# Kernel optimization log

Hardware: AMD Instinct MI355X
Metric: run time of the kernel (lower is better)

The kernel has to match this reference:

```python
import jax, jax.numpy as jnp
import numpy as np

B, S, D = 2, 2048, 1024
H, DK = 16, 64            # n_heads, d_k = d_model // n_heads
EXP = 4                   # pattern-separation expand_factor
ED = DK * EXP             # expanded_dim = 256
TOPK = 32                 # top-k kept after ReLU expansion
ALPHA = 0.05
TNT = 1.0                 # trace_norm_target


def setup_inputs() -> dict:
    key = jax.random.key(0)
    ks = jax.random.split(key, 8)
    sc = 1.0 / np.sqrt(D)
    x = jax.random.normal(ks[0], (B, S, D), jnp.float32)
    W_q = jax.random.normal(ks[1], (D, D), jnp.float32) * sc
    W_k = jax.random.normal(ks[2], (D, D), jnp.float32) * sc
    W_v = jax.random.normal(ks[3], (D, D), jnp.float32) * sc
    W_o = jax.random.normal(ks[4], (D, D), jnp.float32) * sc
    # trace buffers (non-zero so the trace read path actually matters)
    traces = jax.random.normal(ks[5], (H, DK, DK), jnp.float32) * 0.02
    value_traces = jax.random.normal(ks[6], (H, ED, DK), jnp.float32) * 0.02
    # frozen random expansion projection (dentate gyrus), W / sqrt(d_k)
    W_expand = jax.random.normal(ks[7], (DK, ED), jnp.float32) / np.sqrt(DK)
    return dict(x=x, W_q=W_q, W_k=W_k, W_v=W_v, W_o=W_o,
                traces=traces, value_traces=value_traces, W_expand=W_expand)


def _eff_alpha(T):
    # alpha / (1 + ||T_h||_F / trace_norm_target), shape (1, H, 1, 1)
    norms = jnp.sqrt(jnp.sum(T * T, axis=(1, 2)))
    return (ALPHA / (1.0 + norms / TNT)).reshape(1, -1, 1, 1)


def _forward(x, W_q, W_k, W_v, W_o, traces, value_traces, W_expand):
    b, s, d = x.shape
    def proj(W):
        return jnp.einsum('bsd,de->bse', x, W).reshape(b, s, H, DK).transpose(0, 2, 1, 3)
    Q, K, V = proj(W_q), proj(W_k), proj(W_v)  # (B, H, S, DK)

    scores = jnp.einsum('bhqd,bhkd->bhqk', Q, K)
    # score trace bias: alpha_eff * (Q @ T @ K^T)
    QT = jnp.einsum('bhqd,hde->bhqe', Q, traces)
    trace_scores = jnp.einsum('bhqe,bhke->bhqk', QT, K)
    scores = (scores + _eff_alpha(traces) * trace_scores) / np.sqrt(DK)
    A = jax.nn.softmax(scores, axis=-1)
    out = jnp.einsum('bhqk,bhkd->bhqd', A, V)

    # value trace read with use_key_q shift: address with previous token's Q
    Q_addr = jnp.concatenate([jnp.zeros_like(Q[:, :, :1, :]), Q[:, :, :-1, :]], axis=2)
    # pattern separation: frozen random expansion + ReLU + top-k sparsify
    Q_exp = jax.nn.relu(jnp.einsum('bhsd,de->bhse', Q_addr, W_expand))  # (B,H,S,ED)
    kth = jax.lax.top_k(Q_exp, TOPK)[0][..., -1:]
    Q_sparse = jnp.where(Q_exp >= kth, Q_exp, 0.0)  # == scatter of top-k vals (ties at 0 contribute 0)
    stored = jnp.einsum('bhse,hed->bhsd', Q_sparse, value_traces)
    out = out + _eff_alpha(value_traces) * stored

    out = out.transpose(0, 2, 1, 3).reshape(b, s, d)
    return jnp.einsum('bsd,de->bse', out, W_o)


def reference(x, W_q, W_k, W_v, W_o, traces, value_traces, W_expand):
    return _forward(x, W_q, W_k, W_v, W_o, traces, value_traces, W_expand)
```

## Files before the change

kernel.cpp:

```cpp
#include <hip/hip_runtime.h>
#include <stdint.h>

#define Bn 2
#define Sn 2048
#define Dn 1024
#define Hn 16
#define DKn 64
#define EDn 256

typedef __attribute__((ext_vector_type(8))) short bvec8;
typedef __attribute__((ext_vector_type(4))) float fvec4;

#define MFMA(a, b, c) __builtin_amdgcn_mfma_f32_16x16x32_bf16(a, b, c, 0, 0, 0)

__device__ __forceinline__ float b2f(unsigned short u) {
  return __uint_as_float(((unsigned)u) << 16);
}
__device__ __forceinline__ unsigned short f2b(float x) {
  unsigned u = __float_as_uint(x);
  u += 0x7fffu + ((u >> 16) & 1u);
  return (unsigned short)(u >> 16);
}
__device__ __forceinline__ void g2l(const unsigned short* g, unsigned short* l) {
  __builtin_amdgcn_global_load_lds(
      (const __attribute__((address_space(1))) void*)g,
      (__attribute__((address_space(3))) void*)l, 16, 0, 0);
}
__device__ __forceinline__ int dpp_sum16(int x) {
  x += __builtin_amdgcn_update_dpp(0, x, 0x140, 0xf, 0xf, true);
  x += __builtin_amdgcn_update_dpp(0, x, 0x141, 0xf, 0xf, true);
  x += __builtin_amdgcn_update_dpp(0, x, 0x1B, 0xf, 0xf, true);
  x += __builtin_amdgcn_update_dpp(0, x, 0xB1, 0xf, 0xf, true);
  return x;
}
__device__ __forceinline__ unsigned dpp_umax16(unsigned x) {
  unsigned t;
  t = (unsigned)__builtin_amdgcn_update_dpp(0, (int)x, 0x140, 0xf, 0xf, true);
  x = x > t ? x : t;
  t = (unsigned)__builtin_amdgcn_update_dpp(0, (int)x, 0x141, 0xf, 0xf, true);
  x = x > t ? x : t;
  t = (unsigned)__builtin_amdgcn_update_dpp(0, (int)x, 0x1B, 0xf, 0xf, true);
  x = x > t ? x : t;
  t = (unsigned)__builtin_amdgcn_update_dpp(0, (int)x, 0xB1, 0xf, 0xf, true);
  x = x > t ? x : t;
  return x;
}

__global__ __launch_bounds__(256) void k_alphas(
    const float* __restrict__ traces, const float* __restrict__ vtr,
    float* __restrict__ alphas) {
  int blk = blockIdx.x;
  const float* base;
  int n;
  if (blk < 16) { base = traces + blk * DKn * DKn; n = DKn * DKn; }
  else          { base = vtr + (blk - 16) * EDn * DKn; n = EDn * DKn; }
  float s = 0.f;
  for (int i = threadIdx.x; i < n; i += 256) { float v = base[i]; s += v * v; }
  __shared__ float red[256];
  red[threadIdx.x] = s;
  __syncthreads();
  for (int off = 128; off > 0; off >>= 1) {
    if (threadIdx.x < off) red[threadIdx.x] += red[threadIdx.x + off];
    __syncthreads();
  }
  if (threadIdx.x == 0) alphas[blk] = 0.05f / (1.f + sqrtf(red[0]));
}

__global__ __launch_bounds__(256) void k_trW(
    const float* __restrict__ w0, const float* __restrict__ w1,
    const float* __restrict__ w2, const float* __restrict__ w3,
    unsigned short* __restrict__ dst) {
  int z = blockIdx.z;
  const float* src = (z == 0) ? w0 : ((z == 1) ? w1 : ((z == 2) ? w2 : w3));
  unsigned short* d = dst + (size_t)z * Dn * Dn;
  __shared__ unsigned short Tl[64][72];
  int tid = threadIdx.x;
  int k0 = blockIdx.y * 64, n0 = blockIdx.x * 64;
#pragma unroll
  for (int i = 0; i < 4; ++i) {
    int q = tid + 256 * i;
    int kr = q >> 4, c4 = q & 15;
    float4 v = *(const float4*)&src[(size_t)(k0 + kr) * Dn + n0 + 4 * c4];
    ushort4 u;
    u.x = f2b(v.x); u.y = f2b(v.y); u.z = f2b(v.z); u.w = f2b(v.w);
    *(ushort4*)&Tl[kr][4 * c4] = u;
  }
  __syncthreads();
#pragma unroll
  for (int i = 0; i < 4; ++i) {
    int q = tid + 256 * i;
    int nr = q >> 4, c4 = q & 15;
    ushort4 u;
    u.x = Tl[4 * c4 + 0][nr]; u.y = Tl[4 * c4 + 1][nr];
    u.z = Tl[4 * c4 + 2][nr]; u.w = Tl[4 * c4 + 3][nr];
    *(ushort4*)&d[(size_t)(n0 + nr) * Dn + k0 + 4 * c4] = u;
  }
}

__global__ __launch_bounds__(256) void k_mkM(const float* __restrict__ tr,
                                             const float* __restrict__ alph,
                                             unsigned short* __restrict__ Mt) {
  int h = blockIdx.x;
  float a = alph[h] * 0.125f;
  const float* th = tr + (size_t)h * DKn * DKn;
  unsigned short* mh = Mt + (size_t)h * DKn * DKn;
  for (int i = threadIdx.x; i < DKn * DKn; i += 256) {
    int e = i >> 6, k = i & 63;
    float v = a * th[(size_t)k * DKn + e] + ((e == k) ? 0.125f : 0.f);
    mh[i] = f2b(v);
  }
}

__global__ __launch_bounds__(256) void k_trE(const float* __restrict__ Wexp,
                                             unsigned short* __restrict__ WexpT) {
  int e0 = blockIdx.x * 64;
  __shared__ unsigned short Tl[64][72];
  int tid = threadIdx.x;
#pragma unroll
  for (int i = 0; i < 4; ++i) {
    int q = tid + 256 * i;
    int dr = q >> 4, c4 = q & 15;
    float4 v = *(const float4*)&Wexp[(size_t)dr * EDn + e0 + 4 * c4];
    ushort4 u;
    u.x = f2b(v.x); u.y = f2b(v.y); u.z = f2b(v.z); u.w = f2b(v.w);
    *(ushort4*)&Tl[dr][4 * c4] = u;
  }
  __syncthreads();
#pragma unroll
  for (int i = 0; i < 4; ++i) {
    int q = tid + 256 * i;
    int er = q >> 4, c4 = q & 15;
    ushort4 u;
    u.x = Tl[4 * c4 + 0][er]; u.y = Tl[4 * c4 + 1][er];
    u.z = Tl[4 * c4 + 2][er]; u.w = Tl[4 * c4 + 3][er];
    *(ushort4*)&WexpT[(size_t)(e0 + er) * DKn + 4 * c4] = u;
  }
}

__global__ __launch_bounds__(256) void k_trVT(const float* __restrict__ vtr,
                                              unsigned short* __restrict__ VTt) {
  int e0 = blockIdx.x * 64;
  int h = blockIdx.y;
  const float* src = vtr + (size_t)h * EDn * DKn;
  unsigned short* dst = VTt + (size_t)h * DKn * EDn;
  __shared__ unsigned short Tl[64][72];
  int tid = threadIdx.x;
#pragma unroll
  for (int i = 0; i < 4; ++i) {
    int q = tid + 256 * i;
    int er = q >> 4, c4 = q & 15;
    float4 v = *(const float4*)&src[(size_t)(e0 + er) * DKn + 4 * c4];
    ushort4 u;
    u.x = f2b(v.x); u.y = f2b(v.y); u.z = f2b(v.z); u.w = f2b(v.w);
    *(ushort4*)&Tl[er][4 * c4] = u;
  }
  __syncthreads();
#pragma unroll
  for (int i = 0; i < 4; ++i) {
    int q = tid + 256 * i;
    int dr = q >> 4, c4 = q & 15;
    ushort4 u;
    u.x = Tl[4 * c4 + 0][dr]; u.y = Tl[4 * c4 + 1][dr];
    u.z = Tl[4 * c4 + 2][dr]; u.w = Tl[4 * c4 + 3][dr];
    *(ushort4*)&dst[(size_t)dr * EDn + e0 + 4 * c4] = u;
  }
}

__global__ __launch_bounds__(256) void k_xb(const float* __restrict__ x,
                                            unsigned short* __restrict__ xb) {
  size_t i = ((size_t)blockIdx.x * 256 + threadIdx.x) * 4;
  float4 v = *(const float4*)&x[i];
  ushort4 u;
  u.x = f2b(v.x); u.y = f2b(v.y); u.z = f2b(v.z); u.w = f2b(v.w);
  *(ushort4*)&xb[i] = u;
}

template <int MODE>
__global__ __launch_bounds__(256) void k_gemm(
    const unsigned short* __restrict__ Ab, const float* __restrict__ Af,
    const unsigned short* __restrict__ BtBase, unsigned short* __restrict__ Qb,
    unsigned short* __restrict__ Kb, unsigned short* __restrict__ VtOut,
    float* __restrict__ Cout) {
  const int z = (MODE == 0) ? blockIdx.z : 0;
  const unsigned short* Bt = BtBase + (size_t)z * Dn * Dn;
  __shared__ unsigned short As[128 * 32];
  __shared__ unsigned short Bs[128 * 32];
  const int tid = threadIdx.x;
  const int w = tid >> 6, lane = tid & 63, qd = lane >> 4, cc = lane & 15;
  const int m0 = blockIdx.y * 128, n0 = blockIdx.x * 128;
  const int mW = 64 * (w >> 1), nW = 64 * (w & 1);
  const int srow = lane >> 2;
  const int schk = 8 * ((lane & 3) ^ (srow & 3));
  const int r0 = 32 * w + srow, r1 = r0 + 16;
  fvec4 acc[4][4];
#pragma unroll
  for (int i = 0; i < 4; ++i)
#pragma unroll
    for (int j = 0; j < 4; ++j) acc[i][j] = (fvec4){0.f, 0.f, 0.f, 0.f};

  for (int k0 = 0; k0 < Dn; k0 += 32) {
    if (MODE == 0) {
      g2l(&Ab[(size_t)(m0 + r0) * Dn + k0 + schk], &As[1024 * w]);
      g2l(&Ab[(size_t)(m0 + r1) * Dn + k0 + schk], &As[1024 * w + 512]);
    } else {
#pragma unroll
      for (int i = 0; i < 4; ++i) {
        int q = tid + 256 * i;
        int row = q >> 3, c4 = q & 7;
        float4 v = *(const float4*)&Af[(size_t)(m0 + row) * Dn + k0 + 4 * c4];
        ushort4 u;
        u.x = f2b(v.x); u.y = f2b(v.y); u.z = f2b(v.z); u.w = f2b(v.w);
        *(ushort4*)&As[row * 32 + 8 * ((c4 >> 1) ^ (row & 3)) + 4 * (c4 & 1)] =
            u;
      }
    }
    g2l(&Bt[(size_t)(n0 + r0) * Dn + k0 + schk], &Bs[1024 * w]);
    g2l(&Bt[(size_t)(n0 + r1) * Dn + k0 + schk], &Bs[1024 * w + 512]);
    __syncthreads();
    bvec8 af[4], bf[4];
#pragma unroll
    for (int i = 0; i < 4; ++i) {
      int ra = mW + 16 * i + cc;
      af[i] = *(const bvec8*)&As[ra * 32 + 8 * (qd ^ (ra & 3))];
      int rb = nW + 16 * i + cc;
      bf[i] = *(const bvec8*)&Bs[rb * 32 + 8 * (qd ^ (rb & 3))];
    }
#pragma unroll
    for (int i = 0; i < 4; ++i)
#pragma unroll
      for (int j = 0; j < 4; ++j) acc[i][j] = MFMA(af[i], bf[j], acc[i][j]);
    __syncthreads();
  }
#pragma unroll
  for (int i = 0; i < 4; ++i)
#pragma unroll
    for (int j = 0; j < 4; ++j) {
      int rowb = m0 + mW + 16 * i + 4 * qd;
      int col = n0 + nW + 16 * j + cc;
      if (MODE == 0) {
        int b = rowb >> 11, s = rowb & 2047;
        int h = col >> 6, dk = col & 63;
        if (z == 2) {
          ushort4 u;
          u.x = f2b(acc[i][j][0]); u.y = f2b(acc[i][j][1]);
          u.z = f2b(acc[i][j][2]); u.w = f2b(acc[i][j][3]);
          *(ushort4*)&VtOut[(((size_t)(b * Hn + h)) * DKn + dk) * Sn + s] = u;
        } else {
          unsigned short* Cb = (z == 0) ? Qb : Kb;
#pragma unroll
          for (int r = 0; r < 4; ++r)
            Cb[(((size_t)(b * Hn + h)) * Sn + s + r) * DKn + dk] =
                f2b(acc[i][j][r]);
        }
      } else {
#pragma unroll
        for (int r = 0; r < 4; ++r)
          Cout[(size_t)(rowb + r) * Dn + col] = acc[i][j][r];
      }
    }
}

__global__ __launch_bounds__(256, 4) void k_pattsep(
    const unsigned short* __restrict__ Qb,
    const unsigned short* __restrict__ WexpT,
    const unsigned short* __restrict__ VTt,
    const float* __restrict__ alphas, float* __restrict__ AT) {
  __shared__ uint4 Ps4[4][256];
  const int tile = blockIdx.x, bh = blockIdx.y;
  const int b = bh >> 4, h = bh & 15;
  const int tid = threadIdx.x;
  const int w = tid >> 6, lane = tid & 63, qd = lane >> 4, cc = lane & 15;
  const float avt = alphas[16 + h];

  const unsigned short* vtab = VTt + (size_t)h * DKn * EDn;
  unsigned short* Pw = (unsigned short*)Ps4[w];

  const int s0 = tile * 64 + w * 16;
  bvec8 aq0 = {}, aq1 = {};
  const int srow = s0 + cc;
  if (srow > 0) {
    const unsigned short* qp = Qb + ((size_t)bh * Sn + srow - 1) * DKn;
    aq0 = *(const bvec8*)&qp[8 * qd];
    aq1 = *(const bvec8*)&qp[32 + 8 * qd];
  }
  fvec4 E[16];
#pragma unroll
  for (int j = 0; j < 16; ++j) {
    const int e = 16 * j + cc;
    const unsigned short* wr = WexpT + (size_t)e * 64;
    bvec8 b0 = *(const bvec8*)&wr[8 * qd];
    bvec8 b1 = *(const bvec8*)&wr[32 + 8 * qd];
    fvec4 zv = {0.f, 0.f, 0.f, 0.f};
    zv = MFMA(aq0, b0, zv);
    E[j] = MFMA(aq1, b1, zv);
  }
#pragma unroll
  for (int j = 0; j < 16; ++j)
#pragma unroll
    for (int r = 0; r < 4; ++r) E[j][r] = fmaxf(E[j][r], 0.f);

  float thr[4];
#pragma unroll
  for (int r = 0; r < 4; ++r) {
    unsigned mx = 0u;
#pragma unroll
    for (int j = 0; j < 16; ++j) {
      unsigned e = __float_as_uint(E[j][r]);
      mx = mx > e ? mx : e;
    }
    mx = dpp_umax16(mx);
    {
      unsigned o = (unsigned)__shfl_xor((int)mx, 16);
      mx = mx > o ? mx : o;
      o = (unsigned)__shfl_xor((int)mx, 32);
      mx = mx > o ? mx : o;
    }
    int bstart = (mx == 0u) ? -1 : (31 - __clz((int)mx));
    bstart = __builtin_amdgcn_readfirstlane(bstart);
    unsigned cur = 0u;
    bool done = false;
    for (int bit = bstart; bit >= 0; --bit) {
      unsigned cand = cur | (1u << bit);
      float t = __uint_as_float(cand);
      int cnt = 0;
#pragma unroll
      for (int j = 0; j < 16; ++j) cnt += (E[j][r] >= t) ? 1 : 0;
      cnt = dpp_sum16(cnt);
      if (!done && cnt >= 32) {
        cur = cand;
        if (cnt == 32) done = true;
      }
      if (__all(done)) break;
    }
    thr[r] = __uint_as_float(cur);
  }

  fvec4 acc2[4];
#pragma unroll
  for (int j2 = 0; j2 < 4; ++j2) acc2[j2] = (fvec4){0.f, 0.f, 0.f, 0.f};

#pragma unroll
  for (int half = 0; half < 2; ++half) {
#pragma unroll
    for (int j = 0; j < 8; ++j) {
      const int jj = j + 8 * half;
#pragma unroll
      for (int r = 0; r < 4; ++r) {
        float v = E[jj][r];
        bool sel = (v >= thr[r]) && (v > 0.f);
        int row = 4 * qd + r;
        int s = 16 * j + cc;
        int ch = (s >> 3) ^ (row & 7);
        Pw[row * 128 + ch * 8 + (s & 7)] = sel ? f2b(v) : (unsigned short)0;
      }
    }
#pragma unroll
    for (int j2 = 0; j2 < 4; ++j2) {
      const int d = 16 * j2 + cc;
      const unsigned short* vr = vtab + (size_t)d * 256;
#pragma unroll
      for (int c = 0; c < 4; ++c) {
        int cg = 4 * (c + 4 * half) + qd;
        bvec8 bv = *(const bvec8*)&vr[8 * cg];
        int ca = 4 * c + qd;
        bvec8 ap = *(const bvec8*)&Pw[cc * 128 + 8 * (ca ^ (cc & 7))];
        acc2[j2] = MFMA(ap, bv, acc2[j2]);
      }
    }
  }
#pragma unroll
  for (int j2 = 0; j2 < 4; ++j2)
#pragma unroll
    for (int r = 0; r < 4; ++r) {
      int row = s0 + 4 * qd + r;
      AT[((size_t)(b * Sn + row)) * Dn + h * DKn + 16 * j2 + cc] =
          avt * acc2[j2][r];
    }
}

__global__ __launch_bounds__(256, 2) void k_attn(
    const unsigned short* __restrict__ Qb, const unsigned short* __restrict__ Kb,
    const unsigned short* __restrict__ Vt, const unsigned short* __restrict__ Mt,
    float* __restrict__ AT) {
  __shared__ unsigned short Kd[3][64 * 64];
  __shared__ unsigned short Vl[3][64 * 64];
  __shared__ unsigned short Ps[4][32 * 64];
  const int bh = blockIdx.x, qt = blockIdx.y;
  const int b = bh >> 4, h = bh & 15;
  const int tid = threadIdx.x;
  const int w = tid >> 6, lane = tid & 63, qd = lane >> 4, cc = lane & 15;
  const float L2E = 1.4426950408889634f;
  const float NB = 23.083120654223414f;

  const unsigned short* qg = Qb + ((size_t)bh * Sn + qt * 128 + w * 32) * DKn;
  const unsigned short* mh = Mt + (size_t)h * DKn * DKn;
  unsigned short* Pw = Ps[w];
  bvec8 mb0[4], mb1[4];
#pragma unroll
  for (int j = 0; j < 4; ++j) {
    mb0[j] = *(const bvec8*)&mh[(size_t)(16 * j + cc) * DKn + 8 * qd];
    mb1[j] = *(const bvec8*)&mh[(size_t)(16 * j + cc) * DKn + 32 + 8 * qd];
  }
#pragma unroll
  for (int f = 0; f < 2; ++f) {
    bvec8 a0 = *(const bvec8*)&qg[(16 * f + cc) * DKn + 8 * qd];
    bvec8 a1 = *(const bvec8*)&qg[(16 * f + cc) * DKn + 32 + 8 * qd];
#pragma unroll
    for (int j = 0; j < 4; ++j) {
      fvec4 zz = {0.f, 0.f, 0.f, 0.f};
      zz = MFMA(a0, mb0[j], zz);
      zz = MFMA(a1, mb1[j], zz);
#pragma unroll
      for (int r = 0; r < 4; ++r) {
        int qr = 16 * f + 4 * qd + r;
        Pw[qr * 64 + 8 * ((2 * j + (cc >> 3)) ^ (qr & 7)) + (cc & 7)] =
            f2b(zz[r]);
      }
    }
  }
  bvec8 aqA0 = *(const bvec8*)&Pw[cc * 64 + 8 * (qd ^ (cc & 7))];
  bvec8 aqA1 = *(const bvec8*)&Pw[cc * 64 + 8 * ((qd + 4) ^ (cc & 7))];
  bvec8 aqB0 = *(const bvec8*)&Pw[(16 + cc) * 64 + 8 * (qd ^ (cc & 7))];
  bvec8 aqB1 = *(const bvec8*)&Pw[(16 + cc) * 64 + 8 * ((qd + 4) ^ (cc & 7))];

  float lsA = 0.f, lsB = 0.f;
  fvec4 OA[4], OB[4];
#pragma unroll
  for (int j = 0; j < 4; ++j) {
    OA[j] = (fvec4){0.f, 0.f, 0.f, 0.f};
    OB[j] = (fvec4){0.f, 0.f, 0.f, 0.f};
  }

  const int vrow = lane >> 3;
  const int vchk = 8 * ((lane & 7) ^ (vrow & 7));
  const unsigned short* kgb = Kb + (size_t)bh * Sn * DKn;
  const unsigned short* vgb = Vt + (size_t)bh * DKn * Sn;

  __builtin_amdgcn_sched_barrier(0);
#pragma unroll
  for (int p = 0; p < 2; ++p) {
    const unsigned short* kg = kgb + (size_t)p * 64 * DKn;
    g2l(&kg[(size_t)(16 * w + vrow) * 64 + vchk], &Kd[p][1024 * w]);
    g2l(&kg[(size_t)(16 * w + 8 + vrow) * 64 + vchk], &Kd[p][1024 * w + 512]);
    g2l(&vgb[(size_t)(16 * w + vrow) * Sn + p * 64 + vchk], &Vl[p][1024 * w]);
    g2l(&vgb[(size_t)(16 * w + 8 + vrow) * Sn + p * 64 + vchk],
        &Vl[p][1024 * w + 512]);
  }

  const int NT = Sn / 64;
  int buf = 0;
  for (int kt = 0; kt < NT; ++kt) {
    asm volatile("s_waitcnt vmcnt(4)" ::: "memory");
    __builtin_amdgcn_s_barrier();
    if (kt + 2 < NT) {
      int nb = buf + 2;
      if (nb >= 3) nb -= 3;
      const unsigned short* kg = kgb + (size_t)(kt + 2) * 64 * DKn;
      unsigned short* Kn = Kd[nb];
      unsigned short* Vn = Vl[nb];
      g2l(&kg[(size_t)(16 * w + vrow) * 64 + vchk], &Kn[1024 * w]);
      g2l(&kg[(size_t)(16 * w + 8 + vrow) * 64 + vchk], &Kn[1024 * w + 512]);
      g2l(&vgb[(size_t)(16 * w + vrow) * Sn + (kt + 2) * 64 + vchk],
          &Vn[1024 * w]);
      g2l(&vgb[(size_t)(16 * w + 8 + vrow) * Sn + (kt + 2) * 64 + vchk],
          &Vn[1024 * w + 512]);
    }
    __builtin_amdgcn_sched_barrier(0);
    const unsigned short* Kc = Kd[buf];
    const unsigned short* Vc = Vl[buf];
    fvec4 sA[4], sB[4];
#pragma unroll
    for (int j = 0; j < 4; ++j) {
      int rk = 16 * j + cc;
      bvec8 b0 = *(const bvec8*)&Kc[rk * 64 + 8 * (qd ^ (cc & 7))];
      bvec8 b1 = *(const bvec8*)&Kc[rk * 64 + 8 * ((qd + 4) ^ (cc & 7))];
      fvec4 z0 = {0.f, 0.f, 0.f, 0.f};
      z0 = MFMA(b0, aqA0, z0);
      sA[j] = MFMA(b1, aqA1, z0);
      fvec4 z1 = {0.f, 0.f, 0.f, 0.f};
      z1 = MFMA(b0, aqB0, z1);
      sB[j] = MFMA(b1, aqB1, z1);
    }
#pragma unroll
    for (int j = 0; j < 4; ++j) {
      float p0 = __builtin_amdgcn_exp2f(fmaf(sA[j][0], L2E, -NB));
      float p1 = __builtin_amdgcn_exp2f(fmaf(sA[j][1], L2E, -NB));
      float p2 = __builtin_amdgcn_exp2f(fmaf(sA[j][2], L2E, -NB));
      float p3 = __builtin_amdgcn_exp2f(fmaf(sA[j][3], L2E, -NB));
      lsA += (p0 + p1) + (p2 + p3);
      unsigned q01, q23;
      asm("v_cvt_pk_bf16_f32 %0, %1, %2" : "=v"(q01) : "v"(p0), "v"(p1));
      asm("v_cvt_pk_bf16_f32 %0, %1, %2" : "=v"(q23) : "v"(p2), "v"(p3));
      uint2 uu;
      uu.x = q01; uu.y = q23;
      *(uint2*)&Pw[cc * 64 + 4 * ((4 * j + qd) ^ cc)] = uu;
    }
#pragma unroll
    for (int j = 0; j < 4; ++j) {
      float p0 = __builtin_amdgcn_exp2f(fmaf(sB[j][0], L2E, -NB));
      float p1 = __builtin_amdgcn_exp2f(fmaf(sB[j][1], L2E, -NB));
      float p2 = __builtin_amdgcn_exp2f(fmaf(sB[j][2], L2E, -NB));
      float p3 = __builtin_amdgcn_exp2f(fmaf(sB[j][3], L2E, -NB));
      lsB += (p0 + p1) + (p2 + p3);
      unsigned q01, q23;
      asm("v_cvt_pk_bf16_f32 %0, %1, %2" : "=v"(q01) : "v"(p0), "v"(p1));
      asm("v_cvt_pk_bf16_f32 %0, %1, %2" : "=v"(q23) : "v"(p2), "v"(p3));
      uint2 uu;
      uu.x = q01; uu.y = q23;
      *(uint2*)&Pw[(16 + cc) * 64 + 4 * ((4 * j + qd) ^ cc)] = uu;
    }
    union U16 { bvec8 v; uint2 u[2]; } UA0, UA1, UB0, UB1;
    UA0.u[0] = *(const uint2*)&Pw[cc * 64 + 4 * ((2 * qd) ^ cc)];
    UA0.u[1] = *(const uint2*)&Pw[cc * 64 + 4 * ((2 * qd + 1) ^ cc)];
    UA1.u[0] = *(const uint2*)&Pw[cc * 64 + 4 * ((8 + 2 * qd) ^ cc)];
    UA1.u[1] = *(const uint2*)&Pw[cc * 64 + 4 * ((9 + 2 * qd) ^ cc)];
    UB0.u[0] = *(const uint2*)&Pw[(16 + cc) * 64 + 4 * ((2 * qd) ^ cc)];
    UB0.u[1] = *(const uint2*)&Pw[(16 + cc) * 64 + 4 * ((2 * qd + 1) ^ cc)];
    UB1.u[0] = *(const uint2*)&Pw[(16 + cc) * 64 + 4 * ((8 + 2 * qd) ^ cc)];
    UB1.u[1] = *(const uint2*)&Pw[(16 + cc) * 64 + 4 * ((9 + 2 * qd) ^ cc)];
#pragma unroll
    for (int j = 0; j < 4; ++j) {
      int rv = 16 * j + cc;
      bvec8 v0 = *(const bvec8*)&Vc[rv * 64 + 8 * (qd ^ (cc & 7))];
      bvec8 v1 = *(const bvec8*)&Vc[rv * 64 + 8 * ((qd + 4) ^ (cc & 7))];
      OA[j] = MFMA(UA0.v, v0, OA[j]);
      OA[j] = MFMA(UA1.v, v1, OA[j]);
      OB[j] = MFMA(UB0.v, v0, OB[j]);
      OB[j] = MFMA(UB1.v, v1, OB[j]);
    }
    buf = (buf == 2) ? 0 : buf + 1;
  }
  lsA += __shfl_xor(lsA, 16);
  lsA += __shfl_xor(lsA, 32);
  lsB += __shfl_xor(lsB, 16);
  lsB += __shfl_xor(lsB, 32);
  float liA = 1.f / lsA, liB = 1.f / lsB;
  float iA[4], iB[4];
#pragma unroll
  for (int r = 0; r < 4; ++r) {
    iA[r] = __shfl(liA, 4 * qd + r);
    iB[r] = __shfl(liB, 4 * qd + r);
  }
#pragma unroll
  for (int j = 0; j < 4; ++j)
#pragma unroll
    for (int r = 0; r < 4; ++r) {
      int rowA = qt * 128 + w * 32 + 4 * qd + r;
      float* pA = AT + ((size_t)(b * Sn + rowA)) * Dn + h * DKn + 16 * j + cc;
      *pA += OA[j][r] * iA[r];
      float* pB = pA + 16 * (size_t)Dn;
      *pB += OB[j][r] * iB[r];
    }
}

extern "C" void kernel_launch(void* const* d_in, const int* in_sizes, int n_in,
                              void* d_out, int out_size, void* d_ws,
                              size_t ws_size, hipStream_t stream) {
  const float* x = (const float*)d_in[0];
  const float* Wq = (const float*)d_in[1];
  const float* Wk = (const float*)d_in[2];
  const float* Wv = (const float*)d_in[3];
  const float* Wo = (const float*)d_in[4];
  const float* traces = (const float*)d_in[5];
  const float* vtr = (const float*)d_in[6];
  const float* Wexp = (const float*)d_in[7];

  const size_t NQ = (size_t)Bn * Hn * Sn * DKn;
  unsigned short* Qb = (unsigned short*)d_ws;
  unsigned short* Kb = Qb + NQ;
  unsigned short* Vt = Kb + NQ;
  unsigned short* Wt = Vt + NQ;
  unsigned short* Mt = Wt + NQ;
  unsigned short* WexpT = Mt + 65536;
  unsigned short* VTt = WexpT + 16384;
  float* alph = (float*)(VTt + 262144);
  float* AT = alph + 32;
  unsigned short* xb = (unsigned short*)AT;

  k_alphas<<<32, 256, 0, stream>>>(traces, vtr, alph);
  k_trW<<<dim3(16, 16, 4), 256, 0, stream>>>(Wq, Wk, Wv, Wo, Wt);
  k_mkM<<<16, 256, 0, stream>>>(traces, alph, Mt);
  k_trE<<<4, 256, 0, stream>>>(Wexp, WexpT);
  k_trVT<<<dim3(4, 16), 256, 0, stream>>>(vtr, VTt);
  k_xb<<<4096, 256, 0, stream>>>(x, xb);
  k_gemm<0><<<dim3(8, 32, 3), 256, 0, stream>>>(xb, nullptr, Wt, Qb, Kb, Vt,
                                                nullptr);
  k_pattsep<<<dim3(32, 32), 256, 0, stream>>>(Qb, WexpT, VTt, alph, AT);
  k_attn<<<dim3(32, 16), 256, 0, stream>>>(Qb, Kb, Vt, Mt, AT);
  k_gemm<1><<<dim3(8, 32, 1), 256, 0, stream>>>(
      nullptr, AT, Wt + 3 * (size_t)Dn * Dn, nullptr, nullptr, nullptr,
      (float*)d_out);
}
```

Before: 281.4 us.

## Fuse pattern-separation value-trace read into attention kernel prologue

```diff
diff --git a/kernel.cpp b/kernel.cpp
--- a/kernel.cpp
+++ b/kernel.cpp
@@ -260,128 +260,12 @@
     }
 }
 
-__global__ __launch_bounds__(256, 4) void k_pattsep(
-    const unsigned short* __restrict__ Qb,
+__global__ __launch_bounds__(256, 2) void k_attn(
+    const unsigned short* __restrict__ Qb, const unsigned short* __restrict__ Kb,
+    const unsigned short* __restrict__ Vt, const unsigned short* __restrict__ Mt,
     const unsigned short* __restrict__ WexpT,
     const unsigned short* __restrict__ VTt,
     const float* __restrict__ alphas, float* __restrict__ AT) {
-  __shared__ uint4 Ps4[4][256];
-  const int tile = blockIdx.x, bh = blockIdx.y;
-  const int b = bh >> 4, h = bh & 15;
-  const int tid = threadIdx.x;
-  const int w = tid >> 6, lane = tid & 63, qd = lane >> 4, cc = lane & 15;
-  const float avt = alphas[16 + h];
-
-  const unsigned short* vtab = VTt + (size_t)h * DKn * EDn;
-  unsigned short* Pw = (unsigned short*)Ps4[w];
-
-  const int s0 = tile * 64 + w * 16;
-  bvec8 aq0 = {}, aq1 = {};
-  const int srow = s0 + cc;
-  if (srow > 0) {
-    const unsigned short* qp = Qb + ((size_t)bh * Sn + srow - 1) * DKn;
-    aq0 = *(const bvec8*)&qp[8 * qd];
-    aq1 = *(const bvec8*)&qp[32 + 8 * qd];
-  }
-  fvec4 E[16];
-#pragma unroll
-  for (int j = 0; j < 16; ++j) {
-    const int e = 16 * j + cc;
-    const unsigned short* wr = WexpT + (size_t)e * 64;
-    bvec8 b0 = *(const bvec8*)&wr[8 * qd];
-    bvec8 b1 = *(const bvec8*)&wr[32 + 8 * qd];
-    fvec4 zv = {0.f, 0.f, 0.f, 0.f};
-    zv = MFMA(aq0, b0, zv);
-    E[j] = MFMA(aq1, b1, zv);
-  }
-#pragma unroll
-  for (int j = 0; j < 16; ++j)
-#pragma unroll
-    for (int r = 0; r < 4; ++r) E[j][r] = fmaxf(E[j][r], 0.f);
-
-  float thr[4];
-#pragma unroll
-  for (int r = 0; r < 4; ++r) {
-    unsigned mx = 0u;
-#pragma unroll
-    for (int j = 0; j < 16; ++j) {
-      unsigned e = __float_as_uint(E[j][r]);
-      mx = mx > e ? mx : e;
-    }
-    mx = dpp_umax16(mx);
-    {
-      unsigned o = (unsigned)__shfl_xor((int)mx, 16);
-      mx = mx > o ? mx : o;
-      o = (unsigned)__shfl_xor((int)mx, 32);
-      mx = mx > o ? mx : o;
-    }
-    int bstart = (mx == 0u) ? -1 : (31 - __clz((int)mx));
-    bstart = __builtin_amdgcn_readfirstlane(bstart);
-    unsigned cur = 0u;
-    bool done = false;
-    for (int bit = bstart; bit >= 0; --bit) {
-      unsigned cand = cur | (1u << bit);
-      float t = __uint_as_float(cand);
-      int cnt = 0;
-#pragma unroll
-      for (int j = 0; j < 16; ++j) cnt += (E[j][r] >= t) ? 1 : 0;
-      cnt = dpp_sum16(cnt);
-      if (!done && cnt >= 32) {
-        cur = cand;
-        if (cnt == 32) done = true;
-      }
-      if (__all(done)) break;
-    }
-    thr[r] = __uint_as_float(cur);
-  }
-
-  fvec4 acc2[4];
-#pragma unroll
-  for (int j2 = 0; j2 < 4; ++j2) acc2[j2] = (fvec4){0.f, 0.f, 0.f, 0.f};
-
-#pragma unroll
-  for (int half = 0; half < 2; ++half) {
-#pragma unroll
-    for (int j = 0; j < 8; ++j) {
-      const int jj = j + 8 * half;
-#pragma unroll
-      for (int r = 0; r < 4; ++r) {
-        float v = E[jj][r];
-        bool sel = (v >= thr[r]) && (v > 0.f);
-        int row = 4 * qd + r;
-        int s = 16 * j + cc;
-        int ch = (s >> 3) ^ (row & 7);
-        Pw[row * 128 + ch * 8 + (s & 7)] = sel ? f2b(v) : (unsigned short)0;
-      }
-    }
-#pragma unroll
-    for (int j2 = 0; j2 < 4; ++j2) {
-      const int d = 16 * j2 + cc;
-      const unsigned short* vr = vtab + (size_t)d * 256;
-#pragma unroll
-      for (int c = 0; c < 4; ++c) {
-        int cg = 4 * (c + 4 * half) + qd;
-        bvec8 bv = *(const bvec8*)&vr[8 * cg];
-        int ca = 4 * c + qd;
-        bvec8 ap = *(const bvec8*)&Pw[cc * 128 + 8 * (ca ^ (cc & 7))];
-        acc2[j2] = MFMA(ap, bv, acc2[j2]);
-      }
-    }
-  }
-#pragma unroll
-  for (int j2 = 0; j2 < 4; ++j2)
-#pragma unroll
-    for (int r = 0; r < 4; ++r) {
-      int row = s0 + 4 * qd + r;
-      AT[((size_t)(b * Sn + row)) * Dn + h * DKn + 16 * j2 + cc] =
-          avt * acc2[j2][r];
-    }
-}
-
-__global__ __launch_bounds__(256, 2) void k_attn(
-    const unsigned short* __restrict__ Qb, const unsigned short* __restrict__ Kb,
-    const unsigned short* __restrict__ Vt, const unsigned short* __restrict__ Mt,
-    float* __restrict__ AT) {
   __shared__ unsigned short Kd[3][64 * 64];
   __shared__ unsigned short Vl[3][64 * 64];
   __shared__ unsigned short Ps[4][32 * 64];
@@ -391,52 +275,14 @@
   const int w = tid >> 6, lane = tid & 63, qd = lane >> 4, cc = lane & 15;
   const float L2E = 1.4426950408889634f;
   const float NB = 23.083120654223414f;
-
-  const unsigned short* qg = Qb + ((size_t)bh * Sn + qt * 128 + w * 32) * DKn;
-  const unsigned short* mh = Mt + (size_t)h * DKn * DKn;
-  unsigned short* Pw = Ps[w];
-  bvec8 mb0[4], mb1[4];
-#pragma unroll
-  for (int j = 0; j < 4; ++j) {
-    mb0[j] = *(const bvec8*)&mh[(size_t)(16 * j + cc) * DKn + 8 * qd];
-    mb1[j] = *(const bvec8*)&mh[(size_t)(16 * j + cc) * DKn + 32 + 8 * qd];
-  }
-#pragma unroll
-  for (int f = 0; f < 2; ++f) {
-    bvec8 a0 = *(const bvec8*)&qg[(16 * f + cc) * DKn + 8 * qd];
-    bvec8 a1 = *(const bvec8*)&qg[(16 * f + cc) * DKn + 32 + 8 * qd];
-#pragma unroll
-    for (int j = 0; j < 4; ++j) {
-      fvec4 zz = {0.f, 0.f, 0.f, 0.f};
-      zz = MFMA(a0, mb0[j], zz);
-      zz = MFMA(a1, mb1[j], zz);
-#pragma unroll
-      for (int r = 0; r < 4; ++r) {
-        int qr = 16 * f + 4 * qd + r;
-        Pw[qr * 64 + 8 * ((2 * j + (cc >> 3)) ^ (qr & 7)) + (cc & 7)] =
-            f2b(zz[r]);
-      }
-    }
-  }
-  bvec8 aqA0 = *(const bvec8*)&Pw[cc * 64 + 8 * (qd ^ (cc & 7))];
-  bvec8 aqA1 = *(const bvec8*)&Pw[cc * 64 + 8 * ((qd + 4) ^ (cc & 7))];
-  bvec8 aqB0 = *(const bvec8*)&Pw[(16 + cc) * 64 + 8 * (qd ^ (cc & 7))];
-  bvec8 aqB1 = *(const bvec8*)&Pw[(16 + cc) * 64 + 8 * ((qd + 4) ^ (cc & 7))];
-
-  float lsA = 0.f, lsB = 0.f;
-  fvec4 OA[4], OB[4];
-#pragma unroll
-  for (int j = 0; j < 4; ++j) {
-    OA[j] = (fvec4){0.f, 0.f, 0.f, 0.f};
-    OB[j] = (fvec4){0.f, 0.f, 0.f, 0.f};
-  }
+  const float avt = alphas[16 + h];
 
   const int vrow = lane >> 3;
   const int vchk = 8 * ((lane & 7) ^ (vrow & 7));
   const unsigned short* kgb = Kb + (size_t)bh * Sn * DKn;
   const unsigned short* vgb = Vt + (size_t)bh * DKn * Sn;
-
-  __builtin_amdgcn_sched_barrier(0);
+  unsigned short* Pw = Ps[w];
+
 #pragma unroll
   for (int p = 0; p < 2; ++p) {
     const unsigned short* kg = kgb + (size_t)p * 64 * DKn;
@@ -445,6 +291,151 @@
     g2l(&vgb[(size_t)(16 * w + vrow) * Sn + p * 64 + vchk], &Vl[p][1024 * w]);
     g2l(&vgb[(size_t)(16 * w + 8 + vrow) * Sn + p * 64 + vchk],
         &Vl[p][1024 * w + 512]);
+  }
+  __builtin_amdgcn_sched_barrier(0);
+
+  const unsigned short* vtab = VTt + (size_t)h * DKn * EDn;
+  fvec4 psA[4], psB[4];
+#pragma unroll
+  for (int rg = 0; rg < 2; ++rg) {
+    const int s0 = qt * 128 + w * 32 + rg * 16;
+    bvec8 aq0 = {}, aq1 = {};
+    const int srow = s0 + cc;
+    if (srow > 0) {
+      const unsigned short* qp = Qb + ((size_t)bh * Sn + srow - 1) * DKn;
+      aq0 = *(const bvec8*)&qp[8 * qd];
+      aq1 = *(const bvec8*)&qp[32 + 8 * qd];
+    }
+    fvec4 E[16];
+#pragma unroll
+    for (int j = 0; j < 16; ++j) {
+      const int e = 16 * j + cc;
+      const unsigned short* wr = WexpT + (size_t)e * 64;
+      bvec8 b0 = *(const bvec8*)&wr[8 * qd];
+      bvec8 b1 = *(const bvec8*)&wr[32 + 8 * qd];
+      fvec4 zv = {0.f, 0.f, 0.f, 0.f};
+      zv = MFMA(aq0, b0, zv);
+      E[j] = MFMA(aq1, b1, zv);
+    }
+#pragma unroll
+    for (int j = 0; j < 16; ++j)
+#pragma unroll
+      for (int r = 0; r < 4; ++r) E[j][r] = fmaxf(E[j][r], 0.f);
+
+    float thr[4];
+#pragma unroll
+    for (int r = 0; r < 4; ++r) {
+      unsigned mx = 0u;
+#pragma unroll
+      for (int j = 0; j < 16; ++j) {
+        unsigned e = __float_as_uint(E[j][r]);
+        mx = mx > e ? mx : e;
+      }
+      mx = dpp_umax16(mx);
+      {
+        unsigned o = (unsigned)__shfl_xor((int)mx, 16);
+        mx = mx > o ? mx : o;
+        o = (unsigned)__shfl_xor((int)mx, 32);
+        mx = mx > o ? mx : o;
+      }
+      int bstart = (mx == 0u) ? -1 : (31 - __clz((int)mx));
+      bstart = __builtin_amdgcn_readfirstlane(bstart);
+      unsigned cur = 0u;
+      bool done = false;
+      for (int bit = bstart; bit >= 0; --bit) {
+        unsigned cand = cur | (1u << bit);
+        float t = __uint_as_float(cand);
+        int cnt = 0;
+#pragma unroll
+        for (int j = 0; j < 16; ++j) cnt += (E[j][r] >= t) ? 1 : 0;
+        cnt = dpp_sum16(cnt);
+        if (!done && cnt >= 32) {
+          cur = cand;
+          if (cnt == 32) done = true;
+        }
+        if (__all(done)) break;
+      }
+      thr[r] = __uint_as_float(cur);
+    }
+
+    fvec4 acc2[4];
+#pragma unroll
+    for (int j2 = 0; j2 < 4; ++j2) acc2[j2] = (fvec4){0.f, 0.f, 0.f, 0.f};
+
+#pragma unroll
+    for (int half = 0; half < 2; ++half) {
+#pragma unroll
+      for (int j = 0; j < 8; ++j) {
+        const int jj = j + 8 * half;
+#pragma unroll
+        for (int r = 0; r < 4; ++r) {
+          float v = E[jj][r];
+          bool sel = (v >= thr[r]) && (v > 0.f);
+          int row = 4 * qd + r;
+          int s = 16 * j + cc;
+          int ch = (s >> 3) ^ (row & 7);
+          Pw[row * 128 + ch * 8 + (s & 7)] = sel ? f2b(v) : (unsigned short)0;
+        }
+      }
+#pragma unroll
+      for (int j2 = 0; j2 < 4; ++j2) {
+        const int d = 16 * j2 + cc;
+        const unsigned short* vr = vtab + (size_t)d * 256;
+#pragma unroll
+        for (int c = 0; c < 4; ++c) {
+          int cg = 4 * (c + 4 * half) + qd;
+          bvec8 bv = *(const bvec8*)&vr[8 * cg];
+          int ca = 4 * c + qd;
+          bvec8 ap = *(const bvec8*)&Pw[cc * 128 + 8 * (ca ^ (cc & 7))];
+          acc2[j2] = MFMA(ap, bv, acc2[j2]);
+        }
+      }
+    }
+    if (rg == 0) {
+#pragma unroll
+      for (int j2 = 0; j2 < 4; ++j2) psA[j2] = acc2[j2];
+    } else {
+#pragma unroll
+      for (int j2 = 0; j2 < 4; ++j2) psB[j2] = acc2[j2];
+    }
+  }
+
+  const unsigned short* qg = Qb + ((size_t)bh * Sn + qt * 128 + w * 32) * DKn;
+  const unsigned short* mh = Mt + (size_t)h * DKn * DKn;
+  bvec8 mb0[4], mb1[4];
+#pragma unroll
+  for (int j = 0; j < 4; ++j) {
+    mb0[j] = *(const bvec8*)&mh[(size_t)(16 * j + cc) * DKn + 8 * qd];
+    mb1[j] = *(const bvec8*)&mh[(size_t)(16 * j + cc) * DKn + 32 + 8 * qd];
+  }
+#pragma unroll
+  for (int f = 0; f < 2; ++f) {
+    bvec8 a0 = *(const bvec8*)&qg[(16 * f + cc) * DKn + 8 * qd];
+    bvec8 a1 = *(const bvec8*)&qg[(16 * f + cc) * DKn + 32 + 8 * qd];
+#pragma unroll
+    for (int j = 0; j < 4; ++j) {
+      fvec4 zz = {0.f, 0.f, 0.f, 0.f};
+      zz = MFMA(a0, mb0[j], zz);
+      zz = MFMA(a1, mb1[j], zz);
+#pragma unroll
+      for (int r = 0; r < 4; ++r) {
+        int qr = 16 * f + 4 * qd + r;
+        Pw[qr * 64 + 8 * ((2 * j + (cc >> 3)) ^ (qr & 7)) + (cc & 7)] =
+            f2b(zz[r]);
+      }
+    }
+  }
+  bvec8 aqA0 = *(const bvec8*)&Pw[cc * 64 + 8 * (qd ^ (cc & 7))];
+  bvec8 aqA1 = *(const bvec8*)&Pw[cc * 64 + 8 * ((qd + 4) ^ (cc & 7))];
+  bvec8 aqB0 = *(const bvec8*)&Pw[(16 + cc) * 64 + 8 * (qd ^ (cc & 7))];
+  bvec8 aqB1 = *(const bvec8*)&Pw[(16 + cc) * 64 + 8 * ((qd + 4) ^ (cc & 7))];
+
+  float lsA = 0.f, lsB = 0.f;
+  fvec4 OA[4], OB[4];
+#pragma unroll
+  for (int j = 0; j < 4; ++j) {
+    OA[j] = (fvec4){0.f, 0.f, 0.f, 0.f};
+    OB[j] = (fvec4){0.f, 0.f, 0.f, 0.f};
   }
 
   const int NT = Sn / 64;
@@ -547,9 +538,9 @@
     for (int r = 0; r < 4; ++r) {
       int rowA = qt * 128 + w * 32 + 4 * qd + r;
       float* pA = AT + ((size_t)(b * Sn + rowA)) * Dn + h * DKn + 16 * j + cc;
-      *pA += OA[j][r] * iA[r];
+      *pA = avt * psA[j][r] + OA[j][r] * iA[r];
       float* pB = pA + 16 * (size_t)Dn;
-      *pB += OB[j][r] * iB[r];
+      *pB = avt * psB[j][r] + OB[j][r] * iB[r];
     }
 }
 
@@ -585,8 +576,8 @@
   k_xb<<<4096, 256, 0, stream>>>(x, xb);
   k_gemm<0><<<dim3(8, 32, 3), 256, 0, stream>>>(xb, nullptr, Wt, Qb, Kb, Vt,
                                                 nullptr);
-  k_pattsep<<<dim3(32, 32), 256, 0, stream>>>(Qb, WexpT, VTt, alph, AT);
-  k_attn<<<dim3(32, 16), 256, 0, stream>>>(Qb, Kb, Vt, Mt, AT);
+  k_attn<<<dim3(32, 16), 256, 0, stream>>>(Qb, Kb, Vt, Mt, WexpT, VTt, alph,
+                                           AT);
   k_gemm<1><<<dim3(8, 32, 1), 256, 0, stream>>>(
       nullptr, AT, Wt + 3 * (size_t)Dn * Dn, nullptr, nullptr, nullptr,
       (float*)d_out);
```

New measurement: 281.8 us. About the same (+0.1%).

## Double-buffer LDS tiles in QKV projection GEMM to overlap loads with MFMA

Applied to the files above, without the earlier changes.

```diff
diff --git a/kernel.cpp b/kernel.cpp
--- a/kernel.cpp
+++ b/kernel.cpp
@@ -183,8 +183,8 @@
     float* __restrict__ Cout) {
   const int z = (MODE == 0) ? blockIdx.z : 0;
   const unsigned short* Bt = BtBase + (size_t)z * Dn * Dn;
-  __shared__ unsigned short As[128 * 32];
-  __shared__ unsigned short Bs[128 * 32];
+  __shared__ unsigned short As[2][128 * 32];
+  __shared__ unsigned short Bs[2][128 * 32];
   const int tid = threadIdx.x;
   const int w = tid >> 6, lane = tid & 63, qd = lane >> 4, cc = lane & 15;
   const int m0 = blockIdx.y * 128, n0 = blockIdx.x * 128;
@@ -198,11 +198,41 @@
 #pragma unroll
     for (int j = 0; j < 4; ++j) acc[i][j] = (fvec4){0.f, 0.f, 0.f, 0.f};
 
-  for (int k0 = 0; k0 < Dn; k0 += 32) {
-    if (MODE == 0) {
-      g2l(&Ab[(size_t)(m0 + r0) * Dn + k0 + schk], &As[1024 * w]);
-      g2l(&Ab[(size_t)(m0 + r1) * Dn + k0 + schk], &As[1024 * w + 512]);
-    } else {
+  if (MODE == 0) {
+    g2l(&Ab[(size_t)(m0 + r0) * Dn + schk], &As[0][1024 * w]);
+    g2l(&Ab[(size_t)(m0 + r1) * Dn + schk], &As[0][1024 * w + 512]);
+    g2l(&Bt[(size_t)(n0 + r0) * Dn + schk], &Bs[0][1024 * w]);
+    g2l(&Bt[(size_t)(n0 + r1) * Dn + schk], &Bs[0][1024 * w + 512]);
+    const int NIT = Dn / 32;
+    for (int it = 0; it < NIT; ++it) {
+      const int buf = it & 1;
+      asm volatile("s_waitcnt vmcnt(0)" ::: "memory");
+      __builtin_amdgcn_s_barrier();
+      if (it + 1 < NIT) {
+        const int k0 = (it + 1) * 32;
+        g2l(&Ab[(size_t)(m0 + r0) * Dn + k0 + schk], &As[buf ^ 1][1024 * w]);
+        g2l(&Ab[(size_t)(m0 + r1) * Dn + k0 + schk],
+            &As[buf ^ 1][1024 * w + 512]);
+        g2l(&Bt[(size_t)(n0 + r0) * Dn + k0 + schk], &Bs[buf ^ 1][1024 * w]);
+        g2l(&Bt[(size_t)(n0 + r1) * Dn + k0 + schk],
+            &Bs[buf ^ 1][1024 * w + 512]);
+      }
+      __builtin_amdgcn_sched_barrier(0);
+      bvec8 af[4], bf[4];
+#pragma unroll
+      for (int i = 0; i < 4; ++i) {
+        int ra = mW + 16 * i + cc;
+        af[i] = *(const bvec8*)&As[buf][ra * 32 + 8 * (qd ^ (ra & 3))];
+        int rb = nW + 16 * i + cc;
+        bf[i] = *(const bvec8*)&Bs[buf][rb * 32 + 8 * (qd ^ (rb & 3))];
+      }
+#pragma unroll
+      for (int i = 0; i < 4; ++i)
+#pragma unroll
+        for (int j = 0; j < 4; ++j) acc[i][j] = MFMA(af[i], bf[j], acc[i][j]);
+    }
+  } else {
+    for (int k0 = 0; k0 < Dn; k0 += 32) {
 #pragma unroll
       for (int i = 0; i < 4; ++i) {
         int q = tid + 256 * i;
@@ -210,26 +240,26 @@
         float4 v = *(const float4*)&Af[(size_t)(m0 + row) * Dn + k0 + 4 * c4];
         ushort4 u;
         u.x = f2b(v.x); u.y = f2b(v.y); u.z = f2b(v.z); u.w = f2b(v.w);
-        *(ushort4*)&As[row * 32 + 8 * ((c4 >> 1) ^ (row & 3)) + 4 * (c4 & 1)] =
-            u;
-      }
-    }
-    g2l(&Bt[(size_t)(n0 + r0) * Dn + k0 + schk], &Bs[1024 * w]);
-    g2l(&Bt[(size_t)(n0 + r1) * Dn + k0 + schk], &Bs[1024 * w + 512]);
-    __syncthreads();
-    bvec8 af[4], bf[4];
-#pragma unroll
-    for (int i = 0; i < 4; ++i) {
-      int ra = mW + 16 * i + cc;
-      af[i] = *(const bvec8*)&As[ra * 32 + 8 * (qd ^ (ra & 3))];
-      int rb = nW + 16 * i + cc;
-      bf[i] = *(const bvec8*)&Bs[rb * 32 + 8 * (qd ^ (rb & 3))];
-    }
-#pragma unroll
-    for (int i = 0; i < 4; ++i)
-#pragma unroll
-      for (int j = 0; j < 4; ++j) acc[i][j] = MFMA(af[i], bf[j], acc[i][j]);
-    __syncthreads();
+        *(ushort4*)&As[0][row * 32 + 8 * ((c4 >> 1) ^ (row & 3)) +
+                          4 * (c4 & 1)] = u;
+      }
+      g2l(&Bt[(size_t)(n0 + r0) * Dn + k0 + schk], &Bs[0][1024 * w]);
+      g2l(&Bt[(size_t)(n0 + r1) * Dn + k0 + schk], &Bs[0][1024 * w + 512]);
+      __syncthreads();
+      bvec8 af[4], bf[4];
+#pragma unroll
+      for (int i = 0; i < 4; ++i) {
+        int ra = mW + 16 * i + cc;
+        af[i] = *(const bvec8*)&As[0][ra * 32 + 8 * (qd ^ (ra & 3))];
+        int rb = nW + 16 * i + cc;
+        bf[i] = *(const bvec8*)&Bs[0][rb * 32 + 8 * (qd ^ (rb & 3))];
+      }
+#pragma unroll
+      for (int i = 0; i < 4; ++i)
+#pragma unroll
+        for (int j = 0; j < 4; ++j) acc[i][j] = MFMA(af[i], bf[j], acc[i][j]);
+      __syncthreads();
+    }
   }
 #pragma unroll
   for (int i = 0; i < 4; ++i)
```

Result: no change. 284.0 us (+0.9%).

## Split attention over two key halves and merge partials in output GEMM

Applied to the files above, without the earlier changes.

```diff
diff --git a/kernel.cpp b/kernel.cpp
--- a/kernel.cpp
+++ b/kernel.cpp
@@ -175,12 +175,20 @@
   *(ushort4*)&xb[i] = u;
 }
 
+__global__ __launch_bounds__(256) void k_linv(const float* __restrict__ lbuf,
+                                              float* __restrict__ linv) {
+  const int BHS = Bn * Hn * Sn;
+  int i = blockIdx.x * 256 + threadIdx.x;
+  linv[i] = 1.f / (lbuf[i] + lbuf[BHS + i]);
+}
+
 template <int MODE>
 __global__ __launch_bounds__(256) void k_gemm(
     const unsigned short* __restrict__ Ab, const float* __restrict__ Af,
     const unsigned short* __restrict__ BtBase, unsigned short* __restrict__ Qb,
     unsigned short* __restrict__ Kb, unsigned short* __restrict__ VtOut,
-    float* __restrict__ Cout) {
+    float* __restrict__ Cout, const float* __restrict__ O0g,
+    const float* __restrict__ O1g, const float* __restrict__ linvp) {
   const int z = (MODE == 0) ? blockIdx.z : 0;
   const unsigned short* Bt = BtBase + (size_t)z * Dn * Dn;
   __shared__ unsigned short As[128 * 32];
@@ -207,7 +215,19 @@
       for (int i = 0; i < 4; ++i) {
         int q = tid + 256 * i;
         int row = q >> 3, c4 = q & 7;
-        float4 v = *(const float4*)&Af[(size_t)(m0 + row) * Dn + k0 + 4 * c4];
+        int gr = m0 + row;
+        size_t idx = (size_t)gr * Dn + k0 + 4 * c4;
+        float4 ps = *(const float4*)&Af[idx];
+        float4 o0 = *(const float4*)&O0g[idx];
+        float4 o1 = *(const float4*)&O1g[idx];
+        int bb = gr >> 11, ss = gr & 2047;
+        int hh = (k0 + 4 * c4) >> 6;
+        float li = linvp[(size_t)(bb * Hn + hh) * Sn + ss];
+        float4 v;
+        v.x = fmaf(o0.x + o1.x, li, ps.x);
+        v.y = fmaf(o0.y + o1.y, li, ps.y);
+        v.z = fmaf(o0.z + o1.z, li, ps.z);
+        v.w = fmaf(o0.w + o1.w, li, ps.w);
         ushort4 u;
         u.x = f2b(v.x); u.y = f2b(v.y); u.z = f2b(v.z); u.w = f2b(v.w);
         *(ushort4*)&As[row * 32 + 8 * ((c4 >> 1) ^ (row & 3)) + 4 * (c4 & 1)] =
@@ -378,19 +398,20 @@
     }
 }
 
-__global__ __launch_bounds__(256, 2) void k_attn(
+__global__ __launch_bounds__(256, 3) void k_attn(
     const unsigned short* __restrict__ Qb, const unsigned short* __restrict__ Kb,
     const unsigned short* __restrict__ Vt, const unsigned short* __restrict__ Mt,
-    float* __restrict__ AT) {
-  __shared__ unsigned short Kd[3][64 * 64];
-  __shared__ unsigned short Vl[3][64 * 64];
+    float* __restrict__ Oacc, float* __restrict__ lbuf) {
+  __shared__ unsigned short Kd[2][64 * 64];
+  __shared__ unsigned short Vl[2][64 * 64];
   __shared__ unsigned short Ps[4][32 * 64];
-  const int bh = blockIdx.x, qt = blockIdx.y;
+  const int bh = blockIdx.x, qt = blockIdx.y, ks = blockIdx.z;
   const int b = bh >> 4, h = bh & 15;
   const int tid = threadIdx.x;
   const int w = tid >> 6, lane = tid & 63, qd = lane >> 4, cc = lane & 15;
   const float L2E = 1.4426950408889634f;
   const float NB = 23.083120654223414f;
+  const int kt0 = ks * 16;
 
   const unsigned short* qg = Qb + ((size_t)bh * Sn + qt * 128 + w * 32) * DKn;
   const unsigned short* mh = Mt + (size_t)h * DKn * DKn;
@@ -437,32 +458,29 @@
   const unsigned short* vgb = Vt + (size_t)bh * DKn * Sn;
 
   __builtin_amdgcn_sched_barrier(0);
-#pragma unroll
-  for (int p = 0; p < 2; ++p) {
-    const unsigned short* kg = kgb + (size_t)p * 64 * DKn;
-    g2l(&kg[(size_t)(16 * w + vrow) * 64 + vchk], &Kd[p][1024 * w]);
-    g2l(&kg[(size_t)(16 * w + 8 + vrow) * 64 + vchk], &Kd[p][1024 * w + 512]);
-    g2l(&vgb[(size_t)(16 * w + vrow) * Sn + p * 64 + vchk], &Vl[p][1024 * w]);
-    g2l(&vgb[(size_t)(16 * w + 8 + vrow) * Sn + p * 64 + vchk],
-        &Vl[p][1024 * w + 512]);
-  }
-
-  const int NT = Sn / 64;
-  int buf = 0;
-  for (int kt = 0; kt < NT; ++kt) {
-    asm volatile("s_waitcnt vmcnt(4)" ::: "memory");
+  {
+    const unsigned short* kg = kgb + (size_t)kt0 * 64 * DKn;
+    g2l(&kg[(size_t)(16 * w + vrow) * 64 + vchk], &Kd[0][1024 * w]);
+    g2l(&kg[(size_t)(16 * w + 8 + vrow) * 64 + vchk], &Kd[0][1024 * w + 512]);
+    g2l(&vgb[(size_t)(16 * w + vrow) * Sn + kt0 * 64 + vchk], &Vl[0][1024 * w]);
+    g2l(&vgb[(size_t)(16 * w + 8 + vrow) * Sn + kt0 * 64 + vchk],
+        &Vl[0][1024 * w + 512]);
+  }
+
+  const int NTs = 16;
+  for (int kt = 0; kt < NTs; ++kt) {
+    const int buf = kt & 1;
+    asm volatile("s_waitcnt vmcnt(0)" ::: "memory");
     __builtin_amdgcn_s_barrier();
-    if (kt + 2 < NT) {
-      int nb = buf + 2;
-      if (nb >= 3) nb -= 3;
-      const unsigned short* kg = kgb + (size_t)(kt + 2) * 64 * DKn;
-      unsigned short* Kn = Kd[nb];
-      unsigned short* Vn = Vl[nb];
+    if (kt + 1 < NTs) {
+      const int gkt = kt0 + kt + 1;
+      const unsigned short* kg = kgb + (size_t)gkt * 64 * DKn;
+      unsigned short* Kn = Kd[buf ^ 1];
+      unsigned short* Vn = Vl[buf ^ 1];
       g2l(&kg[(size_t)(16 * w + vrow) * 64 + vchk], &Kn[1024 * w]);
       g2l(&kg[(size_t)(16 * w + 8 + vrow) * 64 + vchk], &Kn[1024 * w + 512]);
-      g2l(&vgb[(size_t)(16 * w + vrow) * Sn + (kt + 2) * 64 + vchk],
-          &Vn[1024 * w]);
-      g2l(&vgb[(size_t)(16 * w + 8 + vrow) * Sn + (kt + 2) * 64 + vchk],
+      g2l(&vgb[(size_t)(16 * w + vrow) * Sn + gkt * 64 + vchk], &Vn[1024 * w]);
+      g2l(&vgb[(size_t)(16 * w + 8 + vrow) * Sn + gkt * 64 + vchk],
           &Vn[1024 * w + 512]);
     }
     __builtin_amdgcn_sched_barrier(0);
@@ -528,29 +546,27 @@
       OB[j] = MFMA(UB0.v, v0, OB[j]);
       OB[j] = MFMA(UB1.v, v1, OB[j]);
     }
-    buf = (buf == 2) ? 0 : buf + 1;
   }
   lsA += __shfl_xor(lsA, 16);
   lsA += __shfl_xor(lsA, 32);
   lsB += __shfl_xor(lsB, 16);
   lsB += __shfl_xor(lsB, 32);
-  float liA = 1.f / lsA, liB = 1.f / lsB;
-  float iA[4], iB[4];
-#pragma unroll
-  for (int r = 0; r < 4; ++r) {
-    iA[r] = __shfl(liA, 4 * qd + r);
-    iB[r] = __shfl(liB, 4 * qd + r);
-  }
+  float* Op = Oacc + (size_t)ks * ((size_t)Bn * Sn * Dn);
 #pragma unroll
   for (int j = 0; j < 4; ++j)
 #pragma unroll
     for (int r = 0; r < 4; ++r) {
       int rowA = qt * 128 + w * 32 + 4 * qd + r;
-      float* pA = AT + ((size_t)(b * Sn + rowA)) * Dn + h * DKn + 16 * j + cc;
-      *pA += OA[j][r] * iA[r];
-      float* pB = pA + 16 * (size_t)Dn;
-      *pB += OB[j][r] * iB[r];
-    }
+      size_t idx = ((size_t)(b * Sn + rowA)) * Dn + h * DKn + 16 * j + cc;
+      Op[idx] = OA[j][r];
+      Op[idx + 16 * (size_t)Dn] = OB[j][r];
+    }
+  if (lane < 16) {
+    int rb = qt * 128 + w * 32;
+    size_t lix = ((size_t)ks * Bn * Hn + b * Hn + h) * Sn + rb + cc;
+    lbuf[lix] = lsA;
+    lbuf[lix + 16] = lsB;
+  }
 }
 
 extern "C" void kernel_launch(void* const* d_in, const int* in_sizes, int n_in,
@@ -566,6 +582,8 @@
   const float* Wexp = (const float*)d_in[7];
 
   const size_t NQ = (size_t)Bn * Hn * Sn * DKn;
+  const size_t NSD = (size_t)Bn * Sn * Dn;
+  const size_t BHS = (size_t)Bn * Hn * Sn;
   unsigned short* Qb = (unsigned short*)d_ws;
   unsigned short* Kb = Qb + NQ;
   unsigned short* Vt = Kb + NQ;
@@ -575,6 +593,9 @@
   unsigned short* VTt = WexpT + 16384;
   float* alph = (float*)(VTt + 262144);
   float* AT = alph + 32;
+  float* Oacc = AT + NSD;
+  float* lbuf = Oacc + 2 * NSD;
+  float* linv = lbuf + 2 * BHS;
   unsigned short* xb = (unsigned short*)AT;
 
   k_alphas<<<32, 256, 0, stream>>>(traces, vtr, alph);
@@ -584,10 +605,12 @@
   k_trVT<<<dim3(4, 16), 256, 0, stream>>>(vtr, VTt);
   k_xb<<<4096, 256, 0, stream>>>(x, xb);
   k_gemm<0><<<dim3(8, 32, 3), 256, 0, stream>>>(xb, nullptr, Wt, Qb, Kb, Vt,
+                                                nullptr, nullptr, nullptr,
                                                 nullptr);
   k_pattsep<<<dim3(32, 32), 256, 0, stream>>>(Qb, WexpT, VTt, alph, AT);
-  k_attn<<<dim3(32, 16), 256, 0, stream>>>(Qb, Kb, Vt, Mt, AT);
+  k_attn<<<dim3(32, 16, 2), 256, 0, stream>>>(Qb, Kb, Vt, Mt, Oacc, lbuf);
+  k_linv<<<256, 256, 0, stream>>>(lbuf, linv);
   k_gemm<1><<<dim3(8, 32, 1), 256, 0, stream>>>(
       nullptr, AT, Wt + 3 * (size_t)Dn * Dn, nullptr, nullptr, nullptr,
-      (float*)d_out);
-}
+      (float*)d_out, Oacc, Oacc + NSD, linv);
+}
```

New measurement: 313.5 us. 11.4% more time.
